# Performance work log

Measured on AMD Instinct MI355X. Metric: run time of the kernel, lower is better.

Reference implementation:

```python
import jax, jax.numpy as jnp
import numpy as np

RELU_NEG_SLOPE = 0.2

def _gat_layer(x, W, a, src, dst, num_nodes, concat):
    # x: [N, Din]; W: [H, Din, F]; a: [H, 2F]; src/dst: [E]
    H, _, F = W.shape
    proj = jnp.einsum('nd,hdf->nhf', x, W)              # [N, H, F]
    a_self, a_nb = a[:, :F], a[:, F:]                   # [H, F] each
    alpha_self = jnp.einsum('nhf,hf->nh', proj, a_self) # [N, H]
    alpha_nb = jnp.einsum('nhf,hf->nh', proj, a_nb)     # [N, H]
    # edge score: a . [proj_dst || proj_src], dst = center node i, src = neighbor j
    e = jax.nn.leaky_relu(alpha_self[dst] + alpha_nb[src], RELU_NEG_SLOPE)  # [E, H]
    e_max = jax.ops.segment_max(e, dst, num_segments=num_nodes)
    e_exp = jnp.exp(e - e_max[dst])
    denom = jax.ops.segment_sum(e_exp, dst, num_segments=num_nodes)
    w = e_exp / denom[dst]                              # [E, H] softmax per dst node
    msg = proj[src] * w[:, :, None]                     # [E, H, F]
    out = jax.ops.segment_sum(msg, dst, num_segments=num_nodes)  # [N, H, F]
    if concat:
        return out.reshape(num_nodes, H * F)
    return out.mean(axis=1)


def setup_inputs() -> dict:
    key = jax.random.key(0)
    k1, k2, k3, k4, k5, k6 = jax.random.split(key, 6)
    N, Din, F1, H1 = 10000, 128, 64, 8
    Dmid = H1 * F1  # 512
    F2, H2 = 64, 1
    x = jax.random.normal(k1, (N, Din), dtype=jnp.float32)
    edges = jax.random.randint(k2, (2, 80000), 0, N, dtype=jnp.int64)
    W1 = jax.random.normal(k3, (H1, Din, F1), dtype=jnp.float32) / np.sqrt(Din)
    a1 = jax.random.normal(k4, (H1, 2 * F1), dtype=jnp.float32) / np.sqrt(2 * F1)
    W2 = jax.random.normal(k5, (H2, Dmid, F2), dtype=jnp.float32) / np.sqrt(Dmid)
    a2 = jax.random.normal(k6, (H2, 2 * F2), dtype=jnp.float32) / np.sqrt(2 * F2)
    return {"x": x, "edges": edges, "W1": W1, "a1": a1, "W2": W2, "a2": a2}


def reference(x, edges, W1, a1, W2, a2):
    N = x.shape[0]
    loops = jnp.arange(N, dtype=edges.dtype)
    # undirected graph + self loops (Graph.neighborhood adds both directions and self)
    src = jnp.concatenate([edges[0], edges[1], loops])
    dst = jnp.concatenate([edges[1], edges[0], loops])
    h = _gat_layer(x, W1, a1, src, dst, N, concat=True)   # [N, 512]
    h = jax.nn.elu(h)
    out = _gat_layer(h, W2, a2, src, dst, N, concat=False)  # [N, 64]
    return out
```

## Files before the change

kernel.cpp:

```cpp
#include <hip/hip_runtime.h>
#include <hip/hip_fp16.h>

#define RELU_NEG_SLOPE 0.2f

typedef _Float16 half8 __attribute__((ext_vector_type(8)));
typedef float f32x4 __attribute__((ext_vector_type(4)));

__device__ __forceinline__ float leaky(float e) {
    return (e > 0.f) ? e : RELU_NEG_SLOPE * e;
}

__device__ __forceinline__ float elu1(float x) {
    return (x > 0.f) ? x : (__expf(x) - 1.f);
}

__device__ int g_cnt[16384];

__global__ __launch_bounds__(256) void k1_scatter_gemm1(
    const int* __restrict__ edges, int E0,
    const float* __restrict__ W2, __half* __restrict__ W2t, int t2,
    unsigned short* __restrict__ ell, int nscat,
    const float4* __restrict__ x4, const float* __restrict__ W1,
    const float* __restrict__ a1, __half* __restrict__ Cp,
    float* __restrict__ as_, float* __restrict__ an_, int N, int slabN) {
    __shared__ __half Bs[64 * 132];
    if (blockIdx.x < nscat) {
        int i = blockIdx.x * 256 + threadIdx.x;
        if (i < 2 * E0) {
            int s = edges[i];
            int d = (i < E0) ? edges[E0 + i] : edges[i - E0];
            int pos = atomicAdd(&g_cnt[d], 1);
            ell[(d << 6) + pos] = (unsigned short)s;
        } else if (i < 2 * E0 + t2) {
            int j = i - 2 * E0;
            int f = j & 63;
            int d = j >> 6;
            W2t[f * 512 + d] = __float2half(W2[j]);
        }
        return;
    }
    int bid2 = blockIdx.x - nscat;
    const int h = bid2 & 7;
    const int by = bid2 >> 3;

    {
        const float4* W1h = (const float4*)W1 + h * 2048;
        int t = threadIdx.x;
#pragma unroll
        for (int r = 0; r < 8; r++) {
            int j4 = t + r * 256;
            float4 w = W1h[j4];
            int f = (j4 << 2) & 63;
            int d = j4 >> 4;
            Bs[(f + 0) * 132 + d] = __float2half(w.x);
            Bs[(f + 1) * 132 + d] = __float2half(w.y);
            Bs[(f + 2) * 132 + d] = __float2half(w.z);
            Bs[(f + 3) * 132 + d] = __float2half(w.w);
        }
    }
    __syncthreads();

    const int lane = threadIdx.x & 63;
    const int wave = threadIdx.x >> 6;
    const int q = lane >> 4;
    const int l15 = lane & 15;
    const int mrow = by * 64 + wave * 16;

    int arow = mrow + l15;
    if (arow >= N) arow = N - 1;
    const float4* Ar = x4 + (size_t)arow * 32;

    f32x4 acc[4] = {{0.f, 0.f, 0.f, 0.f}, {0.f, 0.f, 0.f, 0.f},
                    {0.f, 0.f, 0.f, 0.f}, {0.f, 0.f, 0.f, 0.f}};
#pragma unroll
    for (int ks = 0; ks < 4; ks++) {
        float4 a0 = Ar[ks * 8 + q * 2];
        float4 a1v = Ar[ks * 8 + q * 2 + 1];
        half8 av;
        av[0] = (_Float16)a0.x; av[1] = (_Float16)a0.y;
        av[2] = (_Float16)a0.z; av[3] = (_Float16)a0.w;
        av[4] = (_Float16)a1v.x; av[5] = (_Float16)a1v.y;
        av[6] = (_Float16)a1v.z; av[7] = (_Float16)a1v.w;
#pragma unroll
        for (int t = 0; t < 4; t++) {
            half8 bv = *(const half8*)(Bs + (t * 16 + l15) * 132 + q * 8 + ks * 32);
            acc[t] = __builtin_amdgcn_mfma_f32_16x16x32_f16(av, bv, acc[t], 0, 0, 0);
        }
    }

    __half* Cs = Cp + (size_t)(h >> 1) * slabN + (h & 1) * 64;
    float asc[4], anc[4];
#pragma unroll
    for (int t = 0; t < 4; t++) {
        asc[t] = a1[h * 128 + t * 16 + l15];
        anc[t] = a1[h * 128 + 64 + t * 16 + l15];
    }
#pragma unroll
    for (int r = 0; r < 4; r++) {
        int mg = mrow + q * 4 + r;
        float ps = 0.f, pn = 0.f;
#pragma unroll
        for (int t = 0; t < 4; t++) {
            float v = acc[t][r];
            ps += v * asc[t];
            pn += v * anc[t];
            if (mg < N)
                Cs[(size_t)mg * 128 + t * 16 + l15] = __float2half(v);
        }
#pragma unroll
        for (int m = 8; m >= 1; m >>= 1) {
            ps += __shfl_xor(ps, m, 64);
            pn += __shfl_xor(pn, m, 64);
        }
        if (l15 == 0 && mg < N) {
            as_[mg * 8 + h] = ps;
            an_[mg * 8 + h] = pn;
        }
    }
}

__global__ __launch_bounds__(256) void agg_h8_sliced(
    const unsigned short* __restrict__ ell,
    const __half* __restrict__ projp, const float* __restrict__ as_,
    const float* __restrict__ an_, __half* __restrict__ outh,
    int N, int slabN) {
    int bid = blockIdx.x;
    int hp = bid & 3;
    int rem = bid >> 2;
    int d = rem * 4 + (threadIdx.x >> 6);
    int lane = threadIdx.x & 63;
    if (d >= N) return;
    const int sub = lane >> 3;
    const int inner = lane & 7;
    const int hh = inner >> 2;
    const int h = hp * 2 + hh;
    const int c16 = (inner & 3) * 16;

    int deg = g_cnt[d];
    const unsigned short* row = ell + (d << 6);
    float asd = as_[d * 8 + h];
    const __half* slab = projp + (size_t)hp * slabN;

    float acc[16];
#pragma unroll
    for (int i = 0; i < 16; i++) acc[i] = 0.f;
    float den = 0.f;
    if (sub == 0) {
        float e = __expf(leaky(asd + an_[d * 8 + h]));
        const __half* p = slab + (size_t)d * 128 + hh * 64 + c16;
        half8 v0 = *(const half8*)p;
        half8 v1 = *(const half8*)(p + 8);
        den = e;
#pragma unroll
        for (int i = 0; i < 8; i++) {
            acc[i] = e * (float)v0[i];
            acc[8 + i] = e * (float)v1[i];
        }
    }
    for (int j0 = 0; j0 < deg; j0 += 8) {
        int j = j0 + sub;
        int jc = (j < deg) ? j : (deg - 1);
        int s = row[jc];
        float e = __expf(leaky(asd + an_[s * 8 + h]));
        if (j >= deg) e = 0.f;
        const __half* p = slab + (size_t)s * 128 + hh * 64 + c16;
        half8 v0 = *(const half8*)p;
        half8 v1 = *(const half8*)(p + 8);
        den += e;
#pragma unroll
        for (int i = 0; i < 8; i++) {
            acc[i] += e * (float)v0[i];
            acc[8 + i] += e * (float)v1[i];
        }
    }

#pragma unroll
    for (int off = 32; off >= 8; off >>= 1) {
#pragma unroll
        for (int i = 0; i < 16; i++) acc[i] += __shfl_down(acc[i], off, 64);
        den += __shfl_down(den, off, 64);
    }

    if (sub == 0) {
        float r = 1.f / den;
        half8 o0, o1;
#pragma unroll
        for (int i = 0; i < 8; i++) {
            o0[i] = (_Float16)elu1(acc[i] * r);
            o1[i] = (_Float16)elu1(acc[8 + i] * r);
        }
        __half* op = outh + (size_t)d * 512 + h * 64 + c16;
        *(half8*)op = o0;
        *(half8*)(op + 8) = o1;
    }
}

__global__ __launch_bounds__(64) void mfma_gemm2(
    const __half* __restrict__ Ah, const __half* __restrict__ Bt,
    const float* __restrict__ a2, __half* __restrict__ Ch,
    float* __restrict__ as_, float* __restrict__ an_, int M) {
    const int lane = threadIdx.x & 63;
    const int q = lane >> 4;
    const int l15 = lane & 15;
    const int mrow = blockIdx.x * 16;

    f32x4 acc[4] = {{0.f, 0.f, 0.f, 0.f}, {0.f, 0.f, 0.f, 0.f},
                    {0.f, 0.f, 0.f, 0.f}, {0.f, 0.f, 0.f, 0.f}};
    const __half* Ap = Ah + (size_t)(mrow + l15) * 512 + q * 8;
    const __half* Bp = Bt + (size_t)l15 * 512 + q * 8;
#pragma unroll
    for (int ks = 0; ks < 16; ks++) {
        half8 av = *(const half8*)(Ap + ks * 32);
#pragma unroll
        for (int t = 0; t < 4; t++) {
            half8 bv = *(const half8*)(Bp + (size_t)t * 16 * 512 + ks * 32);
            acc[t] = __builtin_amdgcn_mfma_f32_16x16x32_f16(av, bv, acc[t], 0, 0, 0);
        }
    }

    float asc[4], anc[4];
#pragma unroll
    for (int t = 0; t < 4; t++) {
        asc[t] = a2[t * 16 + l15];
        anc[t] = a2[64 + t * 16 + l15];
    }
#pragma unroll
    for (int r = 0; r < 4; r++) {
        int mg = mrow + q * 4 + r;
        float ps = 0.f, pn = 0.f;
#pragma unroll
        for (int t = 0; t < 4; t++) {
            float v = acc[t][r];
            ps += v * asc[t];
            pn += v * anc[t];
            if (mg < M)
                Ch[(size_t)mg * 64 + t * 16 + l15] = __float2half(v);
        }
#pragma unroll
        for (int m = 8; m >= 1; m >>= 1) {
            ps += __shfl_xor(ps, m, 64);
            pn += __shfl_xor(pn, m, 64);
        }
        if (l15 == 0 && mg < M) {
            as_[mg] = ps;
            an_[mg] = pn;
        }
    }
}

__global__ __launch_bounds__(256) void agg_node_h1(
    const unsigned short* __restrict__ ell,
    const __half* __restrict__ projh, const float* __restrict__ as_,
    const float* __restrict__ an_, float* __restrict__ out, int N) {
    int d = blockIdx.x * 4 + (threadIdx.x >> 6);
    int lane = threadIdx.x & 63;
    if (d >= N) return;
    int sub = lane >> 3;
    int inner = lane & 7;
    int deg = g_cnt[d];
    if (lane == 0) g_cnt[d] = 0;
    const unsigned short* row = ell + (d << 6);
    float asd = as_[d];

    float acc[8];
#pragma unroll
    for (int i = 0; i < 8; i++) acc[i] = 0.f;
    float den = 0.f;
    for (int j0 = 0; j0 < deg; j0 += 8) {
        int j = j0 + sub;
        int jc = (j < deg) ? j : (deg - 1);
        int s = row[jc];
        float e = __expf(leaky(asd + an_[s]));
        if (j >= deg) e = 0.f;
        half8 v = *(const half8*)(projh + (size_t)s * 64 + inner * 8);
        den += e;
#pragma unroll
        for (int i = 0; i < 8; i++) acc[i] += e * (float)v[i];
    }

#pragma unroll
    for (int off = 32; off >= 8; off >>= 1) {
#pragma unroll
        for (int i = 0; i < 8; i++) acc[i] += __shfl_down(acc[i], off, 64);
        den += __shfl_down(den, off, 64);
    }

    if (sub == 0) {
        float e = __expf(leaky(asd + an_[d]));
        half8 v = *(const half8*)(projh + (size_t)d * 64 + inner * 8);
        den += e;
#pragma unroll
        for (int i = 0; i < 8; i++) acc[i] += e * (float)v[i];
        float rden = 1.f / den;
        float4 r0, r1;
        r0.x = acc[0] * rden; r0.y = acc[1] * rden;
        r0.z = acc[2] * rden; r0.w = acc[3] * rden;
        r1.x = acc[4] * rden; r1.y = acc[5] * rden;
        r1.z = acc[6] * rden; r1.w = acc[7] * rden;
        float* op = out + (size_t)d * 64 + inner * 8;
        *(float4*)op = r0;
        *(float4*)(op + 4) = r1;
    }
}

extern "C" void kernel_launch(void* const* d_in, const int* in_sizes, int n_in,
                              void* d_out, int out_size, void* d_ws, size_t ws_size,
                              hipStream_t stream) {
    const float* x  = (const float*)d_in[0];
    const int* edges = (const int*)d_in[1];
    const float* W1 = (const float*)d_in[2];
    const float* a1 = (const float*)d_in[3];
    const float* W2 = (const float*)d_in[4];
    const float* a2 = (const float*)d_in[5];

    const int Din = 128, H1 = 8, F = 64, Dmid = 512;
    const int N = in_sizes[0] / Din;
    const int E0 = in_sizes[1] / 2;
    const int Mpad = (N + 63) & ~63;
    const int slabN = Mpad * 128;

    char* base = (char*)d_ws;
    size_t off = 0;
    auto take = [&](size_t bytes) {
        void* p = base + off;
        off = (off + bytes + 255) & ~(size_t)255;
        return p;
    };
    __half* proj1p = (__half*)take((size_t)4 * slabN * 2);
    __half* hbufh  = (__half*)take((size_t)Mpad * Dmid * 2);
    __half* proj2h = (__half*)take((size_t)N * F * 2);
    __half* W2t    = (__half*)take((size_t)F * Dmid * 2);
    float* as1 = (float*)take((size_t)N * H1 * 4);
    float* an1 = (float*)take((size_t)N * H1 * 4);
    float* as2 = (float*)take((size_t)N * 4);
    float* an2 = (float*)take((size_t)N * 4);
    unsigned short* ell = (unsigned short*)take((size_t)N * 64 * 2);

    int t2 = Dmid * F;
    int nscat = (2 * E0 + t2 + 255) / 256;
    int ngemm = H1 * (Mpad / 64);
    k1_scatter_gemm1<<<nscat + ngemm, 256, 0, stream>>>(
        edges, E0, W2, W2t, t2, ell, nscat,
        (const float4*)x, W1, a1, proj1p, as1, an1, N, slabN);

    int nbp = (N + 3) / 4;
    agg_h8_sliced<<<4 * nbp, 256, 0, stream>>>(ell, proj1p, as1, an1,
                                               hbufh, N, slabN);

    mfma_gemm2<<<(N + 15) / 16, 64, 0, stream>>>(hbufh, W2t, a2, proj2h,
                                                 as2, an2, N);

    agg_node_h1<<<(N + 3) / 4, 256, 0, stream>>>(ell, proj2h,
                                                 as2, an2, (float*)d_out, N);
}
```

Measured before the change: 133.4 us.

## Fuse layer-1 aggregation with layer-2 GEMM through shared memory

Merges the head-sliced layer-1 aggregation and the layer-2 projection GEMM into one kernel. Each 256-thread block aggregates 16 nodes into an LDS tile, then its four waves each compute a 16-column slice of the GEMM. This removes the global round trip of the hidden [N,512] activation and one kernel launch. Workspace buffers also move to static device globals. The trade-off is that each block walks 16 nodes serially, so there are fewer blocks (about 625) and less parallelism for latency hiding during the gather phase.

```diff
diff --git a/kernel.cpp b/kernel.cpp
--- a/kernel.cpp
+++ b/kernel.cpp
@@ -14,15 +14,24 @@
     return (x > 0.f) ? x : (__expf(x) - 1.f);
 }
 
-__device__ int g_cnt[16384];
+#define MAXN 16384
+#define MAXPAD 16384
+
+__device__ __align__(256) int            g_cnt[MAXN];
+__device__ __align__(256) unsigned short g_ell[MAXN * 64];
+__device__ __align__(256) __half         g_proj1p[(size_t)4 * MAXPAD * 128];
+__device__ __align__(256) __half         g_W2t[64 * 512];
+__device__ __align__(256) __half         g_proj2h[MAXN * 64];
+__device__ __align__(256) float          g_as1[MAXN * 8];
+__device__ __align__(256) float          g_an1[MAXN * 8];
+__device__ __align__(256) float          g_as2[MAXN];
+__device__ __align__(256) float          g_an2[MAXN];
 
 __global__ __launch_bounds__(256) void k1_scatter_gemm1(
     const int* __restrict__ edges, int E0,
-    const float* __restrict__ W2, __half* __restrict__ W2t, int t2,
-    unsigned short* __restrict__ ell, int nscat,
+    const float* __restrict__ W2, int t2, int nscat,
     const float4* __restrict__ x4, const float* __restrict__ W1,
-    const float* __restrict__ a1, __half* __restrict__ Cp,
-    float* __restrict__ as_, float* __restrict__ an_, int N, int slabN) {
+    const float* __restrict__ a1, int N, int slabN) {
     __shared__ __half Bs[64 * 132];
     if (blockIdx.x < nscat) {
         int i = blockIdx.x * 256 + threadIdx.x;
@@ -30,12 +39,12 @@
             int s = edges[i];
             int d = (i < E0) ? edges[E0 + i] : edges[i - E0];
             int pos = atomicAdd(&g_cnt[d], 1);
-            ell[(d << 6) + pos] = (unsigned short)s;
+            g_ell[(d << 6) + pos] = (unsigned short)s;
         } else if (i < 2 * E0 + t2) {
             int j = i - 2 * E0;
             int f = j & 63;
             int d = j >> 6;
-            W2t[f * 512 + d] = __float2half(W2[j]);
+            g_W2t[f * 512 + d] = __float2half(W2[j]);
         }
         return;
     }
@@ -88,7 +97,7 @@
         }
     }
 
-    __half* Cs = Cp + (size_t)(h >> 1) * slabN + (h & 1) * 64;
+    __half* Cs = g_proj1p + (size_t)(h >> 1) * slabN + (h & 1) * 64;
     float asc[4], anc[4];
 #pragma unroll
     for (int t = 0; t < 4; t++) {
@@ -113,145 +122,130 @@
             pn += __shfl_xor(pn, m, 64);
         }
         if (l15 == 0 && mg < N) {
-            as_[mg * 8 + h] = ps;
-            an_[mg * 8 + h] = pn;
-        }
-    }
-}
-
-__global__ __launch_bounds__(256) void agg_h8_sliced(
-    const unsigned short* __restrict__ ell,
-    const __half* __restrict__ projp, const float* __restrict__ as_,
-    const float* __restrict__ an_, __half* __restrict__ outh,
-    int N, int slabN) {
-    int bid = blockIdx.x;
-    int hp = bid & 3;
-    int rem = bid >> 2;
-    int d = rem * 4 + (threadIdx.x >> 6);
-    int lane = threadIdx.x & 63;
-    if (d >= N) return;
+            g_as1[mg * 8 + h] = ps;
+            g_an1[mg * 8 + h] = pn;
+        }
+    }
+}
+
+__global__ __launch_bounds__(256) void k23_agg1_gemm2(
+    const float* __restrict__ a2, int N, int slabN) {
+    __shared__ __half hb[16][520];
+    __shared__ float red[4][16][2];
+    const int node0 = blockIdx.x * 16;
+    const int wave = threadIdx.x >> 6;
+    const int lane = threadIdx.x & 63;
+
+    const int hp = wave;
     const int sub = lane >> 3;
     const int inner = lane & 7;
     const int hh = inner >> 2;
     const int h = hp * 2 + hh;
     const int c16 = (inner & 3) * 16;
-
-    int deg = g_cnt[d];
-    const unsigned short* row = ell + (d << 6);
-    float asd = as_[d * 8 + h];
-    const __half* slab = projp + (size_t)hp * slabN;
-
-    float acc[16];
-#pragma unroll
-    for (int i = 0; i < 16; i++) acc[i] = 0.f;
-    float den = 0.f;
-    if (sub == 0) {
-        float e = __expf(leaky(asd + an_[d * 8 + h]));
-        const __half* p = slab + (size_t)d * 128 + hh * 64 + c16;
-        half8 v0 = *(const half8*)p;
-        half8 v1 = *(const half8*)(p + 8);
-        den = e;
-#pragma unroll
-        for (int i = 0; i < 8; i++) {
-            acc[i] = e * (float)v0[i];
-            acc[8 + i] = e * (float)v1[i];
-        }
-    }
-    for (int j0 = 0; j0 < deg; j0 += 8) {
-        int j = j0 + sub;
-        int jc = (j < deg) ? j : (deg - 1);
-        int s = row[jc];
-        float e = __expf(leaky(asd + an_[s * 8 + h]));
-        if (j >= deg) e = 0.f;
-        const __half* p = slab + (size_t)s * 128 + hh * 64 + c16;
-        half8 v0 = *(const half8*)p;
-        half8 v1 = *(const half8*)(p + 8);
-        den += e;
-#pragma unroll
-        for (int i = 0; i < 8; i++) {
-            acc[i] += e * (float)v0[i];
-            acc[8 + i] += e * (float)v1[i];
-        }
-    }
-
-#pragma unroll
-    for (int off = 32; off >= 8; off >>= 1) {
-#pragma unroll
-        for (int i = 0; i < 16; i++) acc[i] += __shfl_down(acc[i], off, 64);
-        den += __shfl_down(den, off, 64);
-    }
-
-    if (sub == 0) {
-        float r = 1.f / den;
-        half8 o0, o1;
-#pragma unroll
-        for (int i = 0; i < 8; i++) {
-            o0[i] = (_Float16)elu1(acc[i] * r);
-            o1[i] = (_Float16)elu1(acc[8 + i] * r);
-        }
-        __half* op = outh + (size_t)d * 512 + h * 64 + c16;
-        *(half8*)op = o0;
-        *(half8*)(op + 8) = o1;
-    }
-}
-
-__global__ __launch_bounds__(64) void mfma_gemm2(
-    const __half* __restrict__ Ah, const __half* __restrict__ Bt,
-    const float* __restrict__ a2, __half* __restrict__ Ch,
-    float* __restrict__ as_, float* __restrict__ an_, int M) {
-    const int lane = threadIdx.x & 63;
+    const __half* slab = g_proj1p + (size_t)hp * slabN;
+
+    for (int nl = 0; nl < 16; nl++) {
+        int d = node0 + nl;
+        if (d >= N) break;
+        int deg = g_cnt[d];
+        const unsigned short* row = g_ell + (d << 6);
+        float asd = g_as1[d * 8 + h];
+
+        float acc[16];
+#pragma unroll
+        for (int i = 0; i < 16; i++) acc[i] = 0.f;
+        float den = 0.f;
+        if (sub == 0) {
+            float e = __expf(leaky(asd + g_an1[d * 8 + h]));
+            const __half* p = slab + (size_t)d * 128 + hh * 64 + c16;
+            half8 v0 = *(const half8*)p;
+            half8 v1 = *(const half8*)(p + 8);
+            den = e;
+#pragma unroll
+            for (int i = 0; i < 8; i++) {
+                acc[i] = e * (float)v0[i];
+                acc[8 + i] = e * (float)v1[i];
+            }
+        }
+        for (int j0 = 0; j0 < deg; j0 += 8) {
+            int j = j0 + sub;
+            int jc = (j < deg) ? j : (deg - 1);
+            int s = row[jc];
+            float e = __expf(leaky(asd + g_an1[s * 8 + h]));
+            if (j >= deg) e = 0.f;
+            const __half* p = slab + (size_t)s * 128 + hh * 64 + c16;
+            half8 v0 = *(const half8*)p;
+            half8 v1 = *(const half8*)(p + 8);
+            den += e;
+#pragma unroll
+            for (int i = 0; i < 8; i++) {
+                acc[i] += e * (float)v0[i];
+                acc[8 + i] += e * (float)v1[i];
+            }
+        }
+#pragma unroll
+        for (int off = 32; off >= 8; off >>= 1) {
+#pragma unroll
+            for (int i = 0; i < 16; i++) acc[i] += __shfl_down(acc[i], off, 64);
+            den += __shfl_down(den, off, 64);
+        }
+        if (sub == 0) {
+            float r = 1.f / den;
+            half8 o0, o1;
+#pragma unroll
+            for (int i = 0; i < 8; i++) {
+                o0[i] = (_Float16)elu1(acc[i] * r);
+                o1[i] = (_Float16)elu1(acc[8 + i] * r);
+            }
+            __half* op = &hb[nl][h * 64 + c16];
+            *(half8*)op = o0;
+            *(half8*)(op + 8) = o1;
+        }
+    }
+    __syncthreads();
+
     const int q = lane >> 4;
     const int l15 = lane & 15;
-    const int mrow = blockIdx.x * 16;
-
-    f32x4 acc[4] = {{0.f, 0.f, 0.f, 0.f}, {0.f, 0.f, 0.f, 0.f},
-                    {0.f, 0.f, 0.f, 0.f}, {0.f, 0.f, 0.f, 0.f}};
-    const __half* Ap = Ah + (size_t)(mrow + l15) * 512 + q * 8;
-    const __half* Bp = Bt + (size_t)l15 * 512 + q * 8;
+    f32x4 acc2 = {0.f, 0.f, 0.f, 0.f};
+    const __half* Bp = g_W2t + (size_t)(wave * 16 + l15) * 512 + q * 8;
 #pragma unroll
     for (int ks = 0; ks < 16; ks++) {
-        half8 av = *(const half8*)(Ap + ks * 32);
-#pragma unroll
-        for (int t = 0; t < 4; t++) {
-            half8 bv = *(const half8*)(Bp + (size_t)t * 16 * 512 + ks * 32);
-            acc[t] = __builtin_amdgcn_mfma_f32_16x16x32_f16(av, bv, acc[t], 0, 0, 0);
-        }
-    }
-
-    float asc[4], anc[4];
-#pragma unroll
-    for (int t = 0; t < 4; t++) {
-        asc[t] = a2[t * 16 + l15];
-        anc[t] = a2[64 + t * 16 + l15];
-    }
+        half8 av = *(const half8*)&hb[l15][ks * 32 + q * 8];
+        half8 bv = *(const half8*)(Bp + ks * 32);
+        acc2 = __builtin_amdgcn_mfma_f32_16x16x32_f16(av, bv, acc2, 0, 0, 0);
+    }
+    float asc = a2[wave * 16 + l15];
+    float anc = a2[64 + wave * 16 + l15];
 #pragma unroll
     for (int r = 0; r < 4; r++) {
-        int mg = mrow + q * 4 + r;
-        float ps = 0.f, pn = 0.f;
-#pragma unroll
-        for (int t = 0; t < 4; t++) {
-            float v = acc[t][r];
-            ps += v * asc[t];
-            pn += v * anc[t];
-            if (mg < M)
-                Ch[(size_t)mg * 64 + t * 16 + l15] = __float2half(v);
-        }
+        int mg = node0 + q * 4 + r;
+        float v = acc2[r];
+        float ps = v * asc, pn = v * anc;
 #pragma unroll
         for (int m = 8; m >= 1; m >>= 1) {
             ps += __shfl_xor(ps, m, 64);
             pn += __shfl_xor(pn, m, 64);
         }
-        if (l15 == 0 && mg < M) {
-            as_[mg] = ps;
-            an_[mg] = pn;
-        }
-    }
-}
-
-__global__ __launch_bounds__(256) void agg_node_h1(
-    const unsigned short* __restrict__ ell,
-    const __half* __restrict__ projh, const float* __restrict__ as_,
-    const float* __restrict__ an_, float* __restrict__ out, int N) {
+        if (mg < N)
+            g_proj2h[(size_t)mg * 64 + wave * 16 + l15] = __float2half(v);
+        if (l15 == 0) {
+            red[wave][q * 4 + r][0] = ps;
+            red[wave][q * 4 + r][1] = pn;
+        }
+    }
+    __syncthreads();
+    if (threadIdx.x < 16) {
+        int mg = node0 + threadIdx.x;
+        if (mg < N) {
+            int i = threadIdx.x;
+            g_as2[mg] = red[0][i][0] + red[1][i][0] + red[2][i][0] + red[3][i][0];
+            g_an2[mg] = red[0][i][1] + red[1][i][1] + red[2][i][1] + red[3][i][1];
+        }
+    }
+}
+
+__global__ __launch_bounds__(256) void agg_node_h1(float* __restrict__ out,
+                                                   int N) {
     int d = blockIdx.x * 4 + (threadIdx.x >> 6);
     int lane = threadIdx.x & 63;
     if (d >= N) return;
@@ -259,8 +253,8 @@
     int inner = lane & 7;
     int deg = g_cnt[d];
     if (lane == 0) g_cnt[d] = 0;
-    const unsigned short* row = ell + (d << 6);
-    float asd = as_[d];
+    const unsigned short* row = g_ell + (d << 6);
+    float asd = g_as2[d];
 
     float acc[8];
 #pragma unroll
@@ -270,9 +264,9 @@
         int j = j0 + sub;
         int jc = (j < deg) ? j : (deg - 1);
         int s = row[jc];
-        float e = __expf(leaky(asd + an_[s]));
+        float e = __expf(leaky(asd + g_an2[s]));
         if (j >= deg) e = 0.f;
-        half8 v = *(const half8*)(projh + (size_t)s * 64 + inner * 8);
+        half8 v = *(const half8*)(g_proj2h + (size_t)s * 64 + inner * 8);
         den += e;
 #pragma unroll
         for (int i = 0; i < 8; i++) acc[i] += e * (float)v[i];
@@ -286,8 +280,8 @@
     }
 
     if (sub == 0) {
-        float e = __expf(leaky(asd + an_[d]));
-        half8 v = *(const half8*)(projh + (size_t)d * 64 + inner * 8);
+        float e = __expf(leaky(asd + g_an2[d]));
+        half8 v = *(const half8*)(g_proj2h + (size_t)d * 64 + inner * 8);
         den += e;
 #pragma unroll
         for (int i = 0; i < 8; i++) acc[i] += e * (float)v[i];
@@ -318,38 +312,15 @@
     const int E0 = in_sizes[1] / 2;
     const int Mpad = (N + 63) & ~63;
     const int slabN = Mpad * 128;
-
-    char* base = (char*)d_ws;
-    size_t off = 0;
-    auto take = [&](size_t bytes) {
-        void* p = base + off;
-        off = (off + bytes + 255) & ~(size_t)255;
-        return p;
-    };
-    __half* proj1p = (__half*)take((size_t)4 * slabN * 2);
-    __half* hbufh  = (__half*)take((size_t)Mpad * Dmid * 2);
-    __half* proj2h = (__half*)take((size_t)N * F * 2);
-    __half* W2t    = (__half*)take((size_t)F * Dmid * 2);
-    float* as1 = (float*)take((size_t)N * H1 * 4);
-    float* an1 = (float*)take((size_t)N * H1 * 4);
-    float* as2 = (float*)take((size_t)N * 4);
-    float* an2 = (float*)take((size_t)N * 4);
-    unsigned short* ell = (unsigned short*)take((size_t)N * 64 * 2);
+    (void)Dmid; (void)d_ws; (void)ws_size;
 
     int t2 = Dmid * F;
     int nscat = (2 * E0 + t2 + 255) / 256;
     int ngemm = H1 * (Mpad / 64);
     k1_scatter_gemm1<<<nscat + ngemm, 256, 0, stream>>>(
-        edges, E0, W2, W2t, t2, ell, nscat,
-        (const float4*)x, W1, a1, proj1p, as1, an1, N, slabN);
-
-    int nbp = (N + 3) / 4;
-    agg_h8_sliced<<<4 * nbp, 256, 0, stream>>>(ell, proj1p, as1, an1,
-                                               hbufh, N, slabN);
-
-    mfma_gemm2<<<(N + 15) / 16, 64, 0, stream>>>(hbufh, W2t, a2, proj2h,
-                                                 as2, an2, N);
-
-    agg_node_h1<<<(N + 3) / 4, 256, 0, stream>>>(ell, proj2h,
-                                                 as2, an2, (float*)d_out, N);
-}
+        edges, E0, W2, t2, nscat, (const float4*)x, W1, a1, N, slabN);
+
+    k23_agg1_gemm2<<<(N + 15) / 16, 256, 0, stream>>>(a2, N, slabN);
+
+    agg_node_h1<<<(N + 3) / 4, 256, 0, stream>>>((float*)d_out, N);
+}
```

Result: slower. 154.1 us (+15.5%).
